# Kernel optimization log

Hardware: AMD Instinct MI355X
Metric: run time of the kernel (lower is better)

Reference implementation:

```python
import jax, jax.numpy as jnp
import numpy as np

N = 6000      # residues (nodes)
E = 120000    # edges (~20 neighbors per node)
D = 128       # node_embedding_dim
De = 128      # edge_embedding_dim
H = 4         # attention heads
L = 2         # encoder layers
C = 2 * D + De
NB, BMIN, BMAX = 16, 2.0, 22.0  # RBF params


def _ln(x, g, b):
    m = x.mean(-1, keepdims=True)
    v = ((x - m) ** 2).mean(-1, keepdims=True)
    return (x - m) / jnp.sqrt(v + 1e-5) * g + b


def setup_inputs() -> dict:
    key = jax.random.key(0)
    ks = iter(jax.random.split(key, 64))

    def nrm(shape, scale=0.05):
        return jax.random.normal(next(ks), shape, jnp.float32) * scale

    inp = {}
    inp['sequence_indices'] = jax.random.randint(next(ks), (N,), 0, 21)
    inp['edge_index'] = jax.random.randint(next(ks), (2, E), 0, N)
    inp['edge_distances'] = BMIN + (BMAX - BMIN) * jax.random.uniform(next(ks), (E,), jnp.float32)
    # parameters
    inp['seq_embed'] = nrm((21, D), 1.0)
    inp['edge_lin_W'] = nrm((NB, De)); inp['edge_lin_b'] = jnp.zeros((De,), jnp.float32)
    inp['aW_W'] = nrm((L, H, C, D)); inp['aW_b'] = jnp.zeros((L, H, D), jnp.float32)
    inp['aA_W'] = nrm((L, H, D));    inp['aA_b'] = jnp.zeros((L, H), jnp.float32)
    inp['nmlp_W1'] = nrm((L, C, D)); inp['nmlp_b1'] = jnp.zeros((L, D), jnp.float32)
    inp['nmlp_W2'] = nrm((L, D, D)); inp['nmlp_b2'] = jnp.zeros((L, D), jnp.float32)
    inp['nmlp_W3'] = nrm((L, D, D)); inp['nmlp_b3'] = jnp.zeros((L, D), jnp.float32)
    inp['dmlp_W1'] = nrm((L, D, 4 * D)); inp['dmlp_b1'] = jnp.zeros((L, 4 * D), jnp.float32)
    inp['dmlp_W2'] = nrm((L, 4 * D, D)); inp['dmlp_b2'] = jnp.zeros((L, D), jnp.float32)
    inp['emlp_W1'] = nrm((L, C, De));  inp['emlp_b1'] = jnp.zeros((L, De), jnp.float32)
    inp['emlp_W2'] = nrm((L, De, De)); inp['emlp_b2'] = jnp.zeros((L, De), jnp.float32)
    inp['emlp_W3'] = nrm((L, De, De)); inp['emlp_b3'] = jnp.zeros((L, De), jnp.float32)
    inp['aggr_W'] = nrm((L, H * D, D)); inp['aggr_b'] = jnp.zeros((L, D), jnp.float32)
    inp['n1_g'] = jnp.ones((L, D), jnp.float32);  inp['n1_b'] = jnp.zeros((L, D), jnp.float32)
    inp['e_g'] = jnp.ones((L, De), jnp.float32);  inp['e_b'] = jnp.zeros((L, De), jnp.float32)
    return inp


def reference(sequence_indices, edge_index, edge_distances, seq_embed,
              edge_lin_W, edge_lin_b, aW_W, aW_b, aA_W, aA_b,
              nmlp_W1, nmlp_b1, nmlp_W2, nmlp_b2, nmlp_W3, nmlp_b3,
              dmlp_W1, dmlp_b1, dmlp_W2, dmlp_b2,
              emlp_W1, emlp_b1, emlp_W2, emlp_b2, emlp_W3, emlp_b3,
              aggr_W, aggr_b, n1_g, n1_b, e_g, e_b):
    gelu = lambda x: jax.nn.gelu(x, approximate=False)  # torch default GELU is exact erf
    lrelu = lambda x: jnp.where(x > 0, x, 0.2 * x)      # LeakyReLU(0.2)

    nodes = seq_embed[sequence_indices]                  # [N, D]
    mu = jnp.linspace(BMIN, BMAX, NB)
    sig = (BMAX - BMIN) / NB
    rbf = jnp.exp(-(((edge_distances[:, None] - mu) / sig) ** 2)) + 1e-8  # [E, NB]
    eattr = rbf @ edge_lin_W + edge_lin_b                # [E, De]

    src, snk = edge_index[0], edge_index[1]
    n = nodes.shape[0]
    for l in range(L):
        feat = jnp.concatenate([nodes[src], nodes[snk], eattr], axis=1)        # [E, C]
        h = lrelu(jnp.einsum('ec,hcd->ehd', feat, aW_W[l]) + aW_b[l][None])    # [E, H, D]
        scores = jnp.einsum('ehd,hd->eh', h, aA_W[l]) + aA_b[l][None]          # [E, H]
        nupd = gelu(feat @ nmlp_W1[l] + nmlp_b1[l])
        nupd = gelu(nupd @ nmlp_W2[l] + nmlp_b2[l])
        nupd = nupd @ nmlp_W3[l] + nmlp_b3[l]                                   # [E, D]
        # scatter softmax over sink nodes (per head)
        smax = jax.ops.segment_max(scores, snk, num_segments=n)                 # [N, H]
        att = jnp.exp(scores - smax[snk])                                       # [E, H]
        norm = jax.ops.segment_sum(att + 1e-12, snk, num_segments=n)            # [N, H]
        att = att / norm[snk]
        msg = (att[:, :, None] * nupd[:, None, :]).reshape(E, H * D)            # head-major concat
        agg = jax.ops.segment_sum(msg, snk, num_segments=n)                     # [N, H*D]
        upd = agg @ aggr_W[l] + aggr_b[l]                                       # [N, D]
        nodes = _ln(nodes + upd, n1_g[l], n1_b[l])
        dense = gelu(nodes @ dmlp_W1[l] + dmlp_b1[l]) @ dmlp_W2[l] + dmlp_b2[l]
        # faithful to source: node_norm1 reused, residual re-adds attention update
        nodes = _ln(dense + upd, n1_g[l], n1_b[l])
        ef = jnp.concatenate([nodes[src], nodes[snk], eattr], axis=1)
        eu = gelu(ef @ emlp_W1[l] + emlp_b1[l])
        eu = gelu(eu @ emlp_W2[l] + emlp_b2[l])
        eu = eu @ emlp_W3[l] + emlp_b3[l]
        eattr = _ln(eattr + eu, e_g[l], e_b[l])
    return nodes, eattr
```

## Files before the change

kernel.cpp:

```cpp
#include <hip/hip_runtime.h>
#include <stdint.h>

#define NN 6000
#define EE 120000
#define DD 128
#define CC 384
#define HDIM 512
#define OUT_NODES (NN*DD)
#define OUT_TOTAL (NN*DD + EE*DD)
#define NODE_LO (NN*DD)
#define EDGE_LO (EE*DD)

typedef unsigned short u16;
typedef __bf16 bf16x8 __attribute__((ext_vector_type(8)));
typedef float f32x4 __attribute__((ext_vector_type(4)));

union V8 { u16 s[8]; uint4 v; };

__device__ __forceinline__ float bf2f(u16 u){ union{unsigned i; float f;} x; x.i=(unsigned)u<<16; return x.f; }
__device__ __forceinline__ u16 f2bf(float f){ union{unsigned i; float f;} x; x.f=f; unsigned r=(x.i + 0x7fffu + ((x.i>>16)&1u))>>16; return (u16)r; }
__device__ __forceinline__ float gelu_f(float v){ return 0.5f*v*(1.f + erff(v*0.70710678118654752f)); }

__device__ __forceinline__ void stage16(void* l, const void* g) {
#if __has_builtin(__builtin_amdgcn_global_load_lds)
  __builtin_amdgcn_global_load_lds(
      (__attribute__((address_space(1))) void*)g,
      (__attribute__((address_space(3))) void*)l, 16, 0, 0);
#else
  *(uint4*)l = *(const uint4*)g;
#endif
}

__device__ __forceinline__ void mfma_step(const u16* buf, int wm, int wn, int lane,
                                          f32x4 acc[4][4])
{
  const int ml = lane & 15;
  const int qx = ((lane >> 4) ^ ((ml ^ (ml >> 2)) & 3)) & 3;
  bf16x8 a_h[4], a_l[4], v_h[4], v_l[4];
#pragma unroll
  for (int mi = 0; mi < 4; ++mi) {
    int ro = (wm*64 + mi*16 + ml)*32 + qx*8;
    a_h[mi] = *(const bf16x8*)(buf + ro);
    a_l[mi] = *(const bf16x8*)(buf + 4096 + ro);
  }
#pragma unroll
  for (int ni = 0; ni < 4; ++ni) {
    int ro = (wn*64 + ni*16 + ml)*32 + qx*8;
    v_h[ni] = *(const bf16x8*)(buf + 8192 + ro);
    v_l[ni] = *(const bf16x8*)(buf + 12288 + ro);
  }
#pragma unroll
  for (int mi = 0; mi < 4; ++mi)
#pragma unroll
    for (int ni = 0; ni < 4; ++ni) {
      acc[mi][ni] = __builtin_amdgcn_mfma_f32_16x16x32_bf16(a_h[mi], v_l[ni], acc[mi][ni], 0, 0, 0);
      acc[mi][ni] = __builtin_amdgcn_mfma_f32_16x16x32_bf16(a_l[mi], v_h[ni], acc[mi][ni], 0, 0, 0);
      acc[mi][ni] = __builtin_amdgcn_mfma_f32_16x16x32_bf16(a_h[mi], v_h[ni], acc[mi][ni], 0, 0, 0);
    }
}

__device__ __forceinline__ int xswz(int row, int col) {
  return row*128 + (col ^ ((row&3)<<3) ^ (((row>>2)&3)<<4));
}

__device__ __forceinline__ void mfma_stepX(const u16* X0, const u16* X1, const u16* BB,
                                           int t, int wm, int wn, int lane, f32x4 acc[4][4])
{
  const int ml = lane & 15, qq = lane >> 4;
  const int qx = (qq ^ ((ml ^ (ml >> 2)) & 3)) & 3;
  bf16x8 a_h[4], a_l[4], v_h[4], v_l[4];
#pragma unroll
  for (int mi = 0; mi < 4; ++mi) {
    int o = xswz(wm*64 + mi*16 + ml, t*32 + qq*8);
    a_h[mi] = *(const bf16x8*)(X0 + o);
    a_l[mi] = *(const bf16x8*)(X1 + o);
  }
#pragma unroll
  for (int ni = 0; ni < 4; ++ni) {
    int ro = (wn*64 + ni*16 + ml)*32 + qx*8;
    v_h[ni] = *(const bf16x8*)(BB + ro);
    v_l[ni] = *(const bf16x8*)(BB + 4096 + ro);
  }
#pragma unroll
  for (int mi = 0; mi < 4; ++mi)
#pragma unroll
    for (int ni = 0; ni < 4; ++ni) {
      acc[mi][ni] = __builtin_amdgcn_mfma_f32_16x16x32_bf16(a_h[mi], v_l[ni], acc[mi][ni], 0, 0, 0);
      acc[mi][ni] = __builtin_amdgcn_mfma_f32_16x16x32_bf16(a_l[mi], v_h[ni], acc[mi][ni], 0, 0, 0);
      acc[mi][ni] = __builtin_amdgcn_mfma_f32_16x16x32_bf16(a_h[mi], v_h[ni], acc[mi][ni], 0, 0, 0);
    }
}

__device__ __forceinline__ void coop_loadZ_b(
    float* ZT, const u16* __restrict__ Zh, int zld, int zs0, int zn0,
    const int* __restrict__ src, const int* __restrict__ snk,
    const int* __restrict__ csr, int m0, int M, int tid)
{
#pragma unroll
  for (int it = 0; it < 8; ++it) {
    int idx = it*256 + tid;
    int row = idx >> 4, c8 = idx & 15;
    int gm = m0 + row; if (gm > M-1) gm = M-1;
    int e = csr[gm];
    V8 a8, b8;
    a8.v = *(const uint4*)(Zh + (size_t)src[e]*zld + zs0 + c8*8);
    b8.v = *(const uint4*)(Zh + (size_t)snk[e]*zld + zn0 + c8*8);
    int base = (c8*8) ^ (((row>>2)&1)<<4);
    float* d = ZT + row*128 + base;
#pragma unroll
    for (int j = 0; j < 8; ++j) d[j] = bf2f(a8.s[j]) + bf2f(b8.s[j]);
  }
}

__device__ __forceinline__ void scatter_X(f32x4 acc[4][4], const float* bias, int gelu_on,
                                          u16* X0, u16* X1, int tid)
{
  const int lane = tid & 63, cl = lane & 15, qr = (lane>>4)&3;
  const int wm = (tid>>6)&1, wn = (tid>>7)&1;
#pragma unroll
  for (int ni = 0; ni < 4; ++ni) {
    float bv = bias[wn*64 + ni*16 + cl];
#pragma unroll
    for (int mi = 0; mi < 4; ++mi)
#pragma unroll
      for (int rg = 0; rg < 4; ++rg) {
        int row = wm*64 + mi*16 + qr*4 + rg;
        int col = wn*64 + ni*16 + cl;
        float v = acc[mi][ni][rg] + bv;
        if (gelu_on) v = gelu_f(v);
        u16 h = f2bf(v);
        int o = xswz(row, col);
        X0[o] = h; X1[o] = f2bf(v - bf2f(h));
      }
  }
}

__device__ __forceinline__ void epilogue_f32(
    f32x4 acc[4][4], const float* bias, float* Cp, int M, int ldc,
    int m0, int n0, int tid)
{
  const int lane = tid & 63;
  const int wm = (tid>>6)&1, wn = (tid>>7)&1;
  const int rl = wm*64 + ((lane>>4)&3)*4;
  const int cl0 = wn*64 + (lane & 15);
#pragma unroll
  for (int ni = 0; ni < 4; ++ni) {
    int gn = n0 + cl0 + ni*16;
    float bv = bias ? bias[gn] : 0.f;
#pragma unroll
    for (int mi = 0; mi < 4; ++mi)
#pragma unroll
      for (int rg = 0; rg < 4; ++rg) {
        int gm = m0 + rl + mi*16 + rg;
        if (gm < M) Cp[(size_t)gm*ldc + gn] = acc[mi][ni][rg] + bv;
      }
  }
}

__device__ __forceinline__ void epilogue_h1(
    f32x4 acc[4][4], u16* Cp, u16* SM, int M, int ldn, int m0, int n0, int tid)
{
  const int lane = tid & 63, cl = lane & 15, qr = (lane>>4)&3;
  const int wm = (tid>>6)&1, wn = (tid>>7)&1;
#pragma unroll
  for (int mi = 0; mi < 4; ++mi)
#pragma unroll
    for (int ni = 0; ni < 4; ++ni)
#pragma unroll
      for (int rg = 0; rg < 4; ++rg) {
        int row = wm*64 + mi*16 + qr*4 + rg;
        int col = wn*64 + ni*16 + cl;
        SM[row*128 + (col ^ (qr<<4))] = f2bf(acc[mi][ni][rg]);
      }
  __syncthreads();
#pragma unroll
  for (int it = 0; it < 8; ++it) {
    int idx = it*256 + tid;
    int row = idx >> 4, blk = idx & 15;
    uint4 val = *(const uint4*)(SM + row*128 + ((blk*8) ^ (((row>>2)&3)<<4)));
    int gm = m0 + row;
    if (gm < M) *(uint4*)(Cp + (size_t)gm*ldn + n0 + blk*8) = val;
  }
  __syncthreads();
}

__device__ __forceinline__ void epilogue_hl(
    f32x4 acc[4][4], const float* bias, u16* Ch, u16* Cl, u16* SM,
    int M, int ldn, int gelu_on, int m0, int n0, int tid)
{
  const int lane = tid & 63, cl = lane & 15, qr = (lane>>4)&3;
  const int wm = (tid>>6)&1, wn = (tid>>7)&1;
#pragma unroll
  for (int ni = 0; ni < 4; ++ni) {
    float bv = bias[n0 + wn*64 + cl + ni*16];
#pragma unroll
    for (int mi = 0; mi < 4; ++mi)
#pragma unroll
      for (int rg = 0; rg < 4; ++rg) {
        float v = acc[mi][ni][rg] + bv;
        if (gelu_on) v = gelu_f(v);
        acc[mi][ni][rg] = v;
      }
  }
#pragma unroll
  for (int pass = 0; pass < 2; ++pass) {
#pragma unroll
    for (int mi = 0; mi < 4; ++mi)
#pragma unroll
      for (int ni = 0; ni < 4; ++ni)
#pragma unroll
        for (int rg = 0; rg < 4; ++rg) {
          int row = wm*64 + mi*16 + qr*4 + rg;
          int col = wn*64 + ni*16 + cl;
          float v = acc[mi][ni][rg];
          u16 h = f2bf(v);
          u16 w = pass ? f2bf(v - bf2f(h)) : h;
          SM[row*128 + (col ^ (qr<<4))] = w;
        }
    __syncthreads();
    u16* Cp = pass ? Cl : Ch;
#pragma unroll
    for (int it = 0; it < 8; ++it) {
      int idx = it*256 + tid;
      int row = idx >> 4, blk = idx & 15;
      uint4 val = *(const uint4*)(SM + row*128 + ((blk*8) ^ (((row>>2)&3)<<4)));
      int gm = m0 + row;
      if (gm < M) *(uint4*)(Cp + (size_t)gm*ldn + n0 + blk*8) = val;
    }
    __syncthreads();
  }
}

__global__ __launch_bounds__(256) void k_gemm2(
    const u16* A_h, const u16* A_l, int K,
    const u16* __restrict__ Bh, const u16* __restrict__ Bl,
    const float* __restrict__ bias, float* Cf,
    u16* Ch, u16* Cl, int M, int ldc, int epi)
{
  __shared__ __align__(16) u16 SM[2][16384];
  const int tid = threadIdx.x, lane = tid & 63;
  const int m0 = blockIdx.x*128, n0 = blockIdx.y*128;
  const int wm = (tid>>6)&1, wn = (tid>>7)&1;
  const u16* gA[2]; const u16* gAl[2]; const u16* gB[2]; const u16* gBl[2];
#pragma unroll
  for (int r = 0; r < 2; ++r) {
    int c = r*256 + tid, m = c>>2, q = c&3;
    int qs = q ^ ((m ^ (m>>2)) & 3);
    int gl = m0 + m; if (gl > M-1) gl = M-1;
    gA[r]  = A_h + (size_t)gl*K + qs*8;
    gAl[r] = A_l + (size_t)gl*K + qs*8;
    gB[r]  = Bh + (size_t)(n0+m)*K + qs*8;
    gBl[r] = Bl + (size_t)(n0+m)*K + qs*8;
  }
  auto stage = [&](int t, u16* buf) {
    int kt = t*32;
#pragma unroll
    for (int r = 0; r < 2; ++r) {
      int c8 = (r*256 + tid)*8;
      stage16(buf + c8,         gA[r]  + kt);
      stage16(buf + 4096 + c8,  gAl[r] + kt);
      stage16(buf + 8192 + c8,  gB[r]  + kt);
      stage16(buf + 12288 + c8, gBl[r] + kt);
    }
  };
  f32x4 acc[4][4] = {};
  const int nk = K >> 5;
  stage(0, SM[0]);
  for (int t = 0; t < nk; ++t) {
    __syncthreads();
    if (t + 1 < nk) stage(t + 1, SM[(t+1)&1]);
    mfma_step(SM[t&1], wm, wn, lane, acc);
  }
  __syncthreads();
  if (epi == 3)      epilogue_f32(acc, bias, Cf, M, ldc, m0, n0, tid);
  else if (epi == 8) epilogue_h1(acc, Ch, SM[0], M, ldc, m0, n0, tid);
  else               epilogue_hl(acc, bias, Ch, Cl, SM[0], M, ldc, epi == 5, m0, n0, tid);
}

__global__ __launch_bounds__(256) void k_mlp_chain(
    const u16* __restrict__ nodes_h, const u16* __restrict__ eattr_h,
    const int* __restrict__ src, const int* __restrict__ snk,
    const u16* __restrict__ B1h, const u16* __restrict__ B1l, const float* __restrict__ b1,
    const u16* __restrict__ B2h, const u16* __restrict__ B2l, const float* __restrict__ b2,
    const u16* __restrict__ B3h, const u16* __restrict__ B3l, const float* __restrict__ b3,
    u16* __restrict__ Xh, u16* __restrict__ Xl, int M)
{
  __shared__ __align__(16) u16 SM[2][16384];
  __shared__ __align__(16) u16 BB[8192];
  const int tid = threadIdx.x, lane = tid & 63;
  const int m0 = blockIdx.x*128;
  const int wm = (tid>>6)&1, wn = (tid>>7)&1;
  const u16* pr0[2]; const u16* pr1[2]; const u16* pr2[2];
  const u16* gB[2]; const u16* gBl[2];
  int soff[2];
#pragma unroll
  for (int r = 0; r < 2; ++r) {
    int c = r*256 + tid, m = c>>2, q = c&3;
    int qs = q ^ ((m ^ (m>>2)) & 3);
    int gl = m0 + m; if (gl > M-1) gl = M-1;
    pr0[r] = nodes_h + (size_t)src[gl]*DD + qs*8;
    pr1[r] = nodes_h + (size_t)snk[gl]*DD + qs*8;
    pr2[r] = eattr_h + (size_t)gl*DD + qs*8;
    gB[r]  = B1h + (size_t)m*CC + qs*8;
    gBl[r] = B1l + (size_t)m*CC + qs*8;
    soff[r] = m*128 + qs*8;
  }
  auto stage_g = [&](int t, u16* buf) {
    int reg = t >> 2, kk = (t & 3) * 32;
    const int LO = (reg == 2) ? EDGE_LO : NODE_LO;
#pragma unroll
    for (int r = 0; r < 2; ++r) {
      int c8 = (r*256 + tid)*8;
      const u16* g = (reg == 0 ? pr0[r] : reg == 1 ? pr1[r] : pr2[r]) + kk;
      stage16(buf + c8,         g);
      stage16(buf + 4096 + c8,  g + LO);
      stage16(buf + 8192 + c8,  gB[r]  + t*32);
      stage16(buf + 12288 + c8, gBl[r] + t*32);
    }
  };
  auto stageB = [&](const u16* Bh_, const u16* Bl_, int t) {
#pragma unroll
    for (int r = 0; r < 2; ++r) {
      int c8 = (r*256 + tid)*8;
      stage16(BB + c8,        Bh_ + soff[r] + t*32);
      stage16(BB + 4096 + c8, Bl_ + soff[r] + t*32);
    }
  };
  f32x4 acc[4][4] = {};
  stage_g(0, SM[0]);
  for (int t = 0; t < 12; ++t) {
    __syncthreads();
    if (t < 11) stage_g(t + 1, SM[(t+1)&1]);
    mfma_step(SM[t&1], wm, wn, lane, acc);
  }
  __syncthreads();
  scatter_X(acc, b1, 1, (u16*)SM[0], (u16*)SM[1], tid);
  __syncthreads();
#pragma unroll
  for (int mi = 0; mi < 4; ++mi)
#pragma unroll
    for (int ni = 0; ni < 4; ++ni)
#pragma unroll
      for (int rg = 0; rg < 4; ++rg) acc[mi][ni][rg] = 0.f;
  for (int t = 0; t < 4; ++t) {
    stageB(B2h, B2l, t);
    __syncthreads();
    mfma_stepX((const u16*)SM[0], (const u16*)SM[1], BB, t, wm, wn, lane, acc);
    __syncthreads();
  }
  scatter_X(acc, b2, 1, (u16*)SM[0], (u16*)SM[1], tid);
  __syncthreads();
#pragma unroll
  for (int mi = 0; mi < 4; ++mi)
#pragma unroll
    for (int ni = 0; ni < 4; ++ni)
#pragma unroll
      for (int rg = 0; rg < 4; ++rg) acc[mi][ni][rg] = 0.f;
  for (int t = 0; t < 4; ++t) {
    stageB(B3h, B3l, t);
    __syncthreads();
    mfma_stepX((const u16*)SM[0], (const u16*)SM[1], BB, t, wm, wn, lane, acc);
    __syncthreads();
  }
  epilogue_hl(acc, b3, Xh, Xl, (u16*)SM[0], M, 128, 0, m0, 0, tid);
}

__global__ __launch_bounds__(256) void k_score(
    const u16* __restrict__ eattr_h,
    const int* __restrict__ src, const int* __restrict__ snk,
    const int* __restrict__ csr,
    const u16* __restrict__ Bh, const u16* __restrict__ Bl,
    const float* __restrict__ bias,
    const float* __restrict__ aAw, const float* __restrict__ aAb,
    const u16* __restrict__ Zatt,
    float* __restrict__ scores_out, int M)
{
  __shared__ __align__(16) u16 SM[2][16384];
  const int tid = threadIdx.x, lane = tid & 63;
  int p = (blockIdx.x & 7) * 469 + (blockIdx.x >> 3);
  const int bm = p >> 2, bn = p & 3;
  const int m0 = bm*128, n0 = bn*128;
  const int wm = (tid>>6)&1, wn = (tid>>7)&1;
  const u16* pr2[2]; const u16* gB[2]; const u16* gBl[2];
#pragma unroll
  for (int r = 0; r < 2; ++r) {
    int c = r*256 + tid, m = c>>2, q = c&3;
    int qs = q ^ ((m ^ (m>>2)) & 3);
    int gl = m0 + m; if (gl > M-1) gl = M-1;
    int ce = csr[gl];
    pr2[r] = eattr_h + (size_t)ce*DD + qs*8;
    gB[r]  = Bh + (size_t)(n0+m)*DD + qs*8;
    gBl[r] = Bl + (size_t)(n0+m)*DD + qs*8;
  }
  auto stage_s = [&](int t, u16* buf) {
#pragma unroll
    for (int r = 0; r < 2; ++r) {
      int c8 = (r*256 + tid)*8;
      stage16(buf + c8,         pr2[r] + t*32);
      stage16(buf + 4096 + c8,  pr2[r] + EDGE_LO + t*32);
      stage16(buf + 8192 + c8,  gB[r]  + t*32);
      stage16(buf + 12288 + c8, gBl[r] + t*32);
    }
  };
  f32x4 acc[4][4] = {};
  stage_s(0, SM[0]);
  for (int t = 0; t < 4; ++t) {
    __syncthreads();
    if (t < 3) stage_s(t + 1, SM[(t+1)&1]);
    mfma_step(SM[t&1], wm, wn, lane, acc);
  }
  __syncthreads();
  float* ZT = (float*)SM;
  coop_loadZ_b(ZT, Zatt, 1024, n0, 512 + n0, src, snk, csr, m0, M, tid);
  __syncthreads();
  const int cl = lane & 15, qr = (lane>>4)&3;
  float pv[16];
#pragma unroll
  for (int mi = 0; mi < 4; ++mi)
#pragma unroll
    for (int rg = 0; rg < 4; ++rg) {
      int row = wm*64 + mi*16 + qr*4 + rg;
      int s = ((row>>2)&1)<<4;
      float pacc = 0.f;
#pragma unroll
      for (int ni = 0; ni < 4; ++ni) {
        int lc = wn*64 + ni*16 + cl;
        int gn = n0 + lc;
        float v = acc[mi][ni][rg] + bias[gn] + ZT[row*128 + (lc ^ s)];
        v = (v > 0.f) ? v : 0.2f*v;
        pacc += v * aAw[gn];
      }
      pacc += __shfl_xor(pacc, 1, 64); pacc += __shfl_xor(pacc, 2, 64);
      pacc += __shfl_xor(pacc, 4, 64); pacc += __shfl_xor(pacc, 8, 64);
      pv[mi*4 + rg] = pacc;
    }
  __syncthreads();
  float* sred = (float*)SM[0];
#pragma unroll
  for (int mi = 0; mi < 4; ++mi)
#pragma unroll
    for (int rg = 0; rg < 4; ++rg)
      if (cl == 0) sred[wn*128 + wm*64 + mi*16 + qr*4 + rg] = pv[mi*4 + rg];
  __syncthreads();
  if (tid < 128) {
    int gm = m0 + tid;
    if (gm < M) scores_out[(size_t)csr[gm]*4 + bn] = sred[tid] + sred[128 + tid] + aAb[bn];
  }
}

__global__ void k_detect(const u16* __restrict__ d, int n, int* __restrict__ flag) {
  __shared__ int cnt;
  if (threadIdx.x == 0) cnt = 0;
  __syncthreads();
  int c = 0;
  for (int i = threadIdx.x; i < n; i += blockDim.x) {
    int e = (d[i] >> 7) & 0xff;
    if (e >= 0xC0) ++c;
  }
  atomicAdd(&cnt, c);
  __syncthreads();
  if (threadIdx.x == 0) *flag = (cnt > 16) ? 1 : 0;
}

struct ConvDesc { const void* src; float* dst; int n; };
struct ConvArgs { ConvDesc d[30]; };
__global__ void k_conv32(ConvArgs a, const int* __restrict__ flag) {
  ConvDesc de = a.d[blockIdx.y];
  int fp = *flag;
  for (int i = blockIdx.x*256 + threadIdx.x; i < de.n; i += gridDim.x*256)
    de.dst[i] = fp ? ((const float*)de.src)[i] : bf2f(((const u16*)de.src)[i]);
}

struct PackDesc { const float* src; u16* dh; u16* dl; int K, N, sk, sh; };
struct PackArgs { PackDesc d[32]; int n; };
__global__ void k_pack2(PackArgs a) {
  PackDesc de = a.d[blockIdx.y];
  int total = de.K * de.N;
  for (int i = blockIdx.x*256 + threadIdx.x; i < total; i += gridDim.x*256) {
    int k = i / de.N, n = i - k*de.N;
    float x = de.src[(size_t)k*de.sk + (n & 127) + (n >> 7)*de.sh];
    u16 h = f2bf(x);
    de.dh[(size_t)n*de.K + k] = h;
    de.dl[(size_t)n*de.K + k] = f2bf(x - bf2f(h));
  }
}

__global__ void k_init_nodes(const int* __restrict__ seq, const float* __restrict__ emb,
                             float* __restrict__ nodes_f, u16* __restrict__ nh) {
  int i = blockIdx.x*256 + threadIdx.x;
  if (i >= NN*DD) return;
  int n = i >> 7, d = i & 127;
  float v = emb[seq[n]*DD + d];
  nodes_f[i] = v;
  u16 h = f2bf(v); nh[i] = h; nh[NODE_LO + i] = f2bf(v - bf2f(h));
}

__global__ void k_rbf_s(const float* __restrict__ dist, const float* __restrict__ W,
                        const float* __restrict__ b, u16* __restrict__ eh) {
  int e = blockIdx.x, t = threadIdx.x;
  float d = dist[e];
  float acc = b[t];
#pragma unroll
  for (int k = 0; k < 16; ++k) {
    float mu = 2.f + (20.f/15.f)*(float)k;
    float z = (d - mu)*0.8f;
    float r = expf(-z*z) + 1e-8f;
    acc += r*W[k*DD + t];
  }
  size_t idx = (size_t)e*DD + t;
  u16 h = f2bf(acc); eh[idx] = h; eh[(size_t)EDGE_LO + idx] = f2bf(acc - bf2f(h));
}

__global__ void k_hist(const int* __restrict__ snk, int* __restrict__ deg) {
  int e = blockIdx.x*256 + threadIdx.x;
  if (e < EE) atomicAdd(&deg[snk[e]], 1);
}
__global__ void k_scan(const int* __restrict__ deg, int* __restrict__ ptr, int* __restrict__ cursor, int n) {
  __shared__ int buf[1024];
  __shared__ int carry_s;
  int tid = threadIdx.x;
  if (tid == 0) carry_s = 0;
  __syncthreads();
  for (int base = 0; base < n; base += 1024) {
    int i = base + tid;
    int v = (i < n) ? deg[i] : 0;
    buf[tid] = v;
    __syncthreads();
    for (int off = 1; off < 1024; off <<= 1) {
      int t = (tid >= off) ? buf[tid - off] : 0;
      __syncthreads();
      buf[tid] += t;
      __syncthreads();
    }
    int excl = buf[tid] - v;
    int carry = carry_s;
    if (i < n) { ptr[i] = carry + excl; cursor[i] = carry + excl; }
    __syncthreads();
    if (tid == 1023) carry_s = carry + buf[1023];
    __syncthreads();
  }
  if (tid == 0) ptr[n] = carry_s;
}
__global__ void k_scatter(const int* __restrict__ snk, int* __restrict__ cursor, int* __restrict__ csr) {
  int e = blockIdx.x*256 + threadIdx.x;
  if (e < EE) { int p = atomicAdd(&cursor[snk[e]], 1); csr[p] = e; }
}

__global__ void k_softmax(const float* __restrict__ scores, const int* __restrict__ ptr,
                          const int* __restrict__ csr, float* __restrict__ att, int nnodes) {
  int node = blockIdx.x*4 + (threadIdx.x >> 6);
  if (node >= nnodes) return;
  int lane = threadIdx.x & 63;
  int h = lane >> 4, j = lane & 15;
  int b = ptr[node], e = ptr[node+1];
  float mx = -1e30f;
  for (int i = b + j; i < e; i += 16) mx = fmaxf(mx, scores[(size_t)csr[i]*4 + h]);
  mx = fmaxf(mx, __shfl_xor(mx, 1, 64)); mx = fmaxf(mx, __shfl_xor(mx, 2, 64));
  mx = fmaxf(mx, __shfl_xor(mx, 4, 64)); mx = fmaxf(mx, __shfl_xor(mx, 8, 64));
  float s = 0.f;
  for (int i = b + j; i < e; i += 16) s += expf(scores[(size_t)csr[i]*4 + h] - mx);
  s += __shfl_xor(s, 1, 64); s += __shfl_xor(s, 2, 64);
  s += __shfl_xor(s, 4, 64); s += __shfl_xor(s, 8, 64);
  float norm = s + (float)(e - b)*1e-12f;
  float inv = (e > b) ? 1.f/norm : 0.f;
  for (int i = b + j; i < e; i += 16) {
    int ed = csr[i];
    att[(size_t)ed*4 + h] = expf(scores[(size_t)ed*4 + h] - mx)*inv;
  }
}

__global__ void k_aggregate(const float* __restrict__ att,
                            const u16* __restrict__ Xh, const u16* __restrict__ Xl,
                            const int* __restrict__ ptr, const int* __restrict__ csr,
                            u16* __restrict__ agg_h, u16* __restrict__ agg_l) {
  int node = blockIdx.x; int d = threadIdx.x;
  int b = ptr[node], e = ptr[node+1];
  float a0=0.f, a1=0.f, a2=0.f, a3=0.f;
  for (int i = b; i < e; ++i) {
    int ed = csr[i];
    float4 a = *(const float4*)(att + (size_t)ed*4);
    size_t xo = (size_t)ed*DD + d;
    float v = bf2f(Xh[xo]) + bf2f(Xl[xo]);
    a0 += a.x*v; a1 += a.y*v; a2 += a.z*v; a3 += a.w*v;
  }
  size_t o = (size_t)node*HDIM + d;
  float vv[4] = {a0, a1, a2, a3};
#pragma unroll
  for (int h = 0; h < 4; ++h) {
    u16 hi = f2bf(vv[h]);
    agg_h[o + h*128] = hi;
    agg_l[o + h*128] = f2bf(vv[h] - bf2f(hi));
  }
}

__global__ void k_ln_node(float* __restrict__ nodes_f,
                          const float* __restrict__ upd, const float* __restrict__ dense_f,
                          const float* __restrict__ g, const float* __restrict__ b,
                          int mode, int rows, u16* __restrict__ nh) {
  int r = blockIdx.x*4 + (threadIdx.x >> 6);
  if (r >= rows) return;
  int lane = threadIdx.x & 63;
  size_t o = (size_t)r*DD;
  float x0, x1;
  if (mode == 0) { x0 = nodes_f[o+lane]; x1 = nodes_f[o+lane+64]; }
  else           { x0 = dense_f[o+lane]; x1 = dense_f[o+lane+64]; }
  x0 += upd[o+lane]; x1 += upd[o+lane+64];
  float s = x0 + x1;
#pragma unroll
  for (int m = 1; m < 64; m <<= 1) s += __shfl_xor(s, m, 64);
  float mean = s * (1.f/128.f);
  float d0 = x0 - mean, d1 = x1 - mean;
  float vv = d0*d0 + d1*d1;
#pragma unroll
  for (int m = 1; m < 64; m <<= 1) vv += __shfl_xor(vv, m, 64);
  float inv = rsqrtf(vv*(1.f/128.f) + 1e-5f);
  float v0 = d0*inv*g[lane]    + b[lane];
  float v1 = d1*inv*g[lane+64] + b[lane+64];
  nodes_f[o+lane]    = v0;
  nodes_f[o+lane+64] = v1;
  u16 h0 = f2bf(v0), h1 = f2bf(v1);
  nh[o+lane] = h0;    nh[NODE_LO + o+lane]    = f2bf(v0 - bf2f(h0));
  nh[o+lane+64] = h1; nh[NODE_LO + o+lane+64] = f2bf(v1 - bf2f(h1));
}

__global__ void k_ln_edge(const u16* __restrict__ Xh, const u16* __restrict__ Xl,
                          const float* __restrict__ g, const float* __restrict__ b,
                          int rows, u16* __restrict__ eh) {
  int r = blockIdx.x*4 + (threadIdx.x >> 6);
  if (r >= rows) return;
  int lane = threadIdx.x & 63;
  size_t o = (size_t)r*DD;
  float x0 = bf2f(eh[o+lane])    + bf2f(eh[(size_t)EDGE_LO + o+lane])
           + bf2f(Xh[o+lane])    + bf2f(Xl[o+lane]);
  float x1 = bf2f(eh[o+lane+64]) + bf2f(eh[(size_t)EDGE_LO + o+lane+64])
           + bf2f(Xh[o+lane+64]) + bf2f(Xl[o+lane+64]);
  float s = x0 + x1;
#pragma unroll
  for (int m = 1; m < 64; m <<= 1) s += __shfl_xor(s, m, 64);
  float mean = s * (1.f/128.f);
  float d0 = x0 - mean, d1 = x1 - mean;
  float vv = d0*d0 + d1*d1;
#pragma unroll
  for (int m = 1; m < 64; m <<= 1) vv += __shfl_xor(vv, m, 64);
  float inv = rsqrtf(vv*(1.f/128.f) + 1e-5f);
  float v0 = d0*inv*g[lane]    + b[lane];
  float v1 = d1*inv*g[lane+64] + b[lane+64];
  u16 h0 = f2bf(v0), h1 = f2bf(v1);
  eh[o+lane] = h0;    eh[(size_t)EDGE_LO + o+lane]    = f2bf(v0 - bf2f(h0));
  eh[o+lane+64] = h1; eh[(size_t)EDGE_LO + o+lane+64] = f2bf(v1 - bf2f(h1));
}

__global__ void k_finalize(const float* __restrict__ nodes_f, const u16* __restrict__ eh,
                           void* __restrict__ out, const int* __restrict__ flag) {
  int i = blockIdx.x*256 + threadIdx.x;
  if (i >= OUT_TOTAL) return;
  int fp = *flag;
  float v;
  if (i < OUT_NODES) v = nodes_f[i];
  else { int j = i - OUT_NODES; v = bf2f(eh[j]) + bf2f(eh[(size_t)EDGE_LO + j]); }
  if (fp) ((float*)out)[i] = v; else ((u16*)out)[i] = f2bf(v);
}

extern "C" void kernel_launch(void* const* d_in, const int* in_sizes, int n_in,
                              void* d_out, int out_size, void* d_ws, size_t ws_size,
                              hipStream_t stream)
{
  const int* seq_idx = (const int*)d_in[0];
  const int* esrc = (const int*)d_in[1];
  const int* esnk = ((const int*)d_in[1]) + EE;

  char* wsp = (char*)d_ws;
  size_t off = 0;
  auto carve = [&](size_t bytes)->char* {
    char* p = wsp + off; off += (bytes + 255) & ~(size_t)255; return p;
  };
  int* flag       = (int*)carve(256);
  float* nodes_f  = (float*)carve((size_t)NN*DD*4);
  float* upd_f    = (float*)carve((size_t)NN*DD*4);
  float* scores   = (float*)carve((size_t)EE*4*4);
  float* att      = (float*)carve((size_t)EE*4*4);
  float* dense_f  = (float*)carve((size_t)NN*DD*4);
  u16* Zatt       = (u16*)carve((size_t)NN*1024*2);
  u16* wpk_h      = (u16*)carve(557056ULL*2*2);
  u16* wpk_l      = (u16*)carve(557056ULL*2*2);
  int* deg        = (int*)carve((size_t)NN*4);
  int* ptrb       = (int*)carve((size_t)(NN+1)*4);
  int* cursor     = (int*)carve((size_t)NN*4);
  int* csr        = (int*)carve((size_t)EE*4);
  u16* nodes_h    = (u16*)carve((size_t)2*NN*DD*2);
  u16* eattr_h    = (u16*)carve((size_t)2*EE*DD*2);
  u16* X_h        = (u16*)carve((size_t)2*EE*DD*2);
  u16* agg_h      = (u16*)carve((size_t)2*NN*HDIM*2);
  u16* dh_h       = (u16*)carve((size_t)2*NN*HDIM*2);
  u16* X_l   = X_h   + (size_t)EE*DD;
  u16* agg_l = agg_h + (size_t)NN*HDIM;
  u16* dh_l  = dh_h  + (size_t)NN*HDIM;

  static const int FCNT[32] = {0,0,120000,2688,2048,128,393216,1024,1024,8,
    98304,256,32768,256,32768,256, 131072,1024,131072,256,
    98304,256,32768,256,32768,256, 131072,256, 256,256,256,256};
  float* cf[32];
  for (int i = 2; i < 32; ++i) cf[i] = (float*)carve((size_t)FCNT[i]*4);
  (void)ws_size; (void)in_sizes; (void)n_in; (void)out_size;

  k_detect<<<1, 1024, 0, stream>>>((const u16*)d_in[2], 120000, flag);
  ConvArgs ca;
  for (int i = 2; i < 32; ++i) { ca.d[i-2].src = d_in[i]; ca.d[i-2].dst = cf[i]; ca.d[i-2].n = FCNT[i]; }
  hipLaunchKernelGGL(k_conv32, dim3(96, 30), dim3(256), 0, stream, ca, flag);

  const size_t PW_L = 557056;
  PackArgs pa; int nd = 0;
  for (int l = 0; l < 2; ++l) {
    size_t base = l*PW_L;
    auto add = [&](const float* s, size_t doff, int K, int N, int sk, int sh){
      pa.d[nd].src = s; pa.d[nd].dh = wpk_h + doff; pa.d[nd].dl = wpk_l + doff;
      pa.d[nd].K = K; pa.d[nd].N = N; pa.d[nd].sk = sk; pa.d[nd].sh = sh; ++nd; };
    const float* aW = cf[6] + l*196608;
    add(aW,          base + 0,      128, 512, 128, 49152);
    add(aW + 16384,  base + 65536,  128, 512, 128, 49152);
    add(aW + 32768,  base + 131072, 128, 512, 128, 49152);
    add(cf[10] + l*49152, base + 196608, 384, 128, 128, 0);
    add(cf[12] + l*16384, base + 245760, 128, 128, 128, 0);
    add(cf[14] + l*16384, base + 262144, 128, 128, 128, 0);
    add(cf[26] + l*65536, base + 278528, 512, 128, 128, 0);
    add(cf[16] + l*65536, base + 344064, 128, 512, 512, 128);
    add(cf[18] + l*65536, base + 409600, 512, 128, 128, 0);
    add(cf[20] + l*49152, base + 475136, 384, 128, 128, 0);
    add(cf[22] + l*16384, base + 524288, 128, 128, 128, 0);
    add(cf[24] + l*16384, base + 540672, 128, 128, 128, 0);
  }
  pa.n = nd;
  hipLaunchKernelGGL(k_pack2, dim3(256, nd), dim3(256), 0, stream, pa);

  k_init_nodes<<<(NN*DD + 255)/256, 256, 0, stream>>>(seq_idx, cf[3], nodes_f, nodes_h);
  k_rbf_s<<<EE, 128, 0, stream>>>(cf[2], cf[4], cf[5], eattr_h);

  (void)hipMemsetAsync(deg, 0, (size_t)NN*4, stream);
  k_hist<<<(EE + 255)/256, 256, 0, stream>>>(esnk, deg);
  k_scan<<<1, 1024, 0, stream>>>(deg, ptrb, cursor, NN);
  k_scatter<<<(EE + 255)/256, 256, 0, stream>>>(esnk, cursor, csr);

  for (int l = 0; l < 2; ++l) {
    const u16* bh = wpk_h + l*PW_L; const u16* bl = wpk_l + l*PW_L;
    k_gemm2<<<dim3(47, 8), 256, 0, stream>>>(nodes_h, nodes_h + NODE_LO, 128,
        bh + 0, bl + 0, nullptr, nullptr, Zatt, nullptr, NN, 1024, 8);
    k_score<<<dim3(3752), 256, 0, stream>>>(eattr_h, esrc, esnk, csr,
        bh + 131072, bl + 131072, cf[7] + l*512, cf[8] + l*512, cf[9] + l*4,
        Zatt, scores, EE);
    k_mlp_chain<<<dim3(938), 256, 0, stream>>>(nodes_h, eattr_h, esrc, esnk,
        bh + 196608, bl + 196608, cf[11] + l*128,
        bh + 245760, bl + 245760, cf[13] + l*128,
        bh + 262144, bl + 262144, cf[15] + l*128,
        X_h, X_l, EE);
    k_softmax<<<(NN + 3)/4, 256, 0, stream>>>(scores, ptrb, csr, att, NN);
    k_aggregate<<<NN, 128, 0, stream>>>(att, X_h, X_l, ptrb, csr, agg_h, agg_l);
    k_gemm2<<<dim3(47, 1), 256, 0, stream>>>(agg_h, agg_l, 512, bh + 278528, bl + 278528,
        cf[27] + l*128, upd_f, nullptr, nullptr, NN, 128, 3);
    k_ln_node<<<(NN + 3)/4, 256, 0, stream>>>(nodes_f, upd_f, (const float*)nullptr,
        cf[28] + l*128, cf[29] + l*128, 0, NN, nodes_h);
    k_gemm2<<<dim3(47, 4), 256, 0, stream>>>(nodes_h, nodes_h + NODE_LO, 128,
        bh + 344064, bl + 344064, cf[17] + l*512, nullptr, dh_h, dh_l, NN, 512, 5);
    k_gemm2<<<dim3(47, 1), 256, 0, stream>>>(dh_h, dh_l, 512, bh + 409600, bl + 409600,
        cf[19] + l*128, dense_f, nullptr, nullptr, NN, 128, 3);
    k_ln_node<<<(NN + 3)/4, 256, 0, stream>>>(nodes_f, upd_f, dense_f,
        cf[28] + l*128, cf[29] + l*128, 1, NN, nodes_h);
    k_mlp_chain<<<dim3(938), 256, 0, stream>>>(nodes_h, eattr_h, esrc, esnk,
        bh + 475136, bl + 475136, cf[21] + l*128,
        bh + 524288, bl + 524288, cf[23] + l*128,
        bh + 540672, bl + 540672, cf[25] + l*128,
        X_h, X_l, EE);
    k_ln_edge<<<(EE + 3)/4, 256, 0, stream>>>(X_h, X_l,
        cf[30] + l*128, cf[31] + l*128, EE, eattr_h);
  }
  k_finalize<<<(OUT_TOTAL + 255)/256, 256, 0, stream>>>(nodes_f, eattr_h, d_out, flag);
}
```

Baseline: 1.175 ms.

## Fuse edge LayerNorm into MLP chain epilogue and read small weights from global

New measurement: 1.247 ms. 6.1% more time.

```diff
diff --git a/kernel.cpp b/kernel.cpp
--- a/kernel.cpp
+++ b/kernel.cpp
@@ -63,23 +63,23 @@
   return row*128 + (col ^ ((row&3)<<3) ^ (((row>>2)&3)<<4));
 }
 
-__device__ __forceinline__ void mfma_stepX(const u16* X0, const u16* X1, const u16* BB,
-                                           int t, int wm, int wn, int lane, f32x4 acc[4][4])
+__device__ __forceinline__ void mfma_stepXg(const u16* X0, const u16* X1,
+    const u16* __restrict__ Bh, const u16* __restrict__ Bl,
+    int t, int wm, int wn, int lane, f32x4 acc[4][4])
 {
   const int ml = lane & 15, qq = lane >> 4;
-  const int qx = (qq ^ ((ml ^ (ml >> 2)) & 3)) & 3;
   bf16x8 a_h[4], a_l[4], v_h[4], v_l[4];
+#pragma unroll
+  for (int ni = 0; ni < 4; ++ni) {
+    size_t ro = (size_t)(wn*64 + ni*16 + ml)*128 + t*32 + qq*8;
+    v_h[ni] = *(const bf16x8*)(Bh + ro);
+    v_l[ni] = *(const bf16x8*)(Bl + ro);
+  }
 #pragma unroll
   for (int mi = 0; mi < 4; ++mi) {
     int o = xswz(wm*64 + mi*16 + ml, t*32 + qq*8);
     a_h[mi] = *(const bf16x8*)(X0 + o);
     a_l[mi] = *(const bf16x8*)(X1 + o);
-  }
-#pragma unroll
-  for (int ni = 0; ni < 4; ++ni) {
-    int ro = (wn*64 + ni*16 + ml)*32 + qx*8;
-    v_h[ni] = *(const bf16x8*)(BB + ro);
-    v_l[ni] = *(const bf16x8*)(BB + 4096 + ro);
   }
 #pragma unroll
   for (int mi = 0; mi < 4; ++mi)
@@ -228,6 +228,54 @@
       if (gm < M) *(uint4*)(Cp + (size_t)gm*ldn + n0 + blk*8) = val;
     }
     __syncthreads();
+  }
+}
+
+__device__ __forceinline__ void epilogue_lnedge(
+    f32x4 acc[4][4], const float* bias, const float* g, const float* b,
+    u16* eh, float* SMf, int M, int m0, int tid)
+{
+  const int lane = tid & 63, cl = lane & 15, qr = (lane>>4)&3;
+  const int wm = (tid>>6)&1, wn = (tid>>7)&1;
+#pragma unroll
+  for (int ni = 0; ni < 4; ++ni) {
+    float bv = bias[wn*64 + ni*16 + cl];
+#pragma unroll
+    for (int mi = 0; mi < 4; ++mi)
+#pragma unroll
+      for (int rg = 0; rg < 4; ++rg) {
+        int row = wm*64 + mi*16 + qr*4 + rg;
+        int col = wn*64 + ni*16 + cl;
+        SMf[row*128 + (col ^ (((row>>2)&1)<<4))] = acc[mi][ni][rg] + bv;
+      }
+  }
+  __syncthreads();
+  const int wid = tid >> 6;
+  float gl0 = g[lane], gl1 = g[lane+64], bl0 = b[lane], bl1 = b[lane+64];
+  for (int rr = 0; rr < 32; ++rr) {
+    int row = wid*32 + rr;
+    int gm = m0 + row;
+    if (gm >= M) break;
+    int s = ((row>>2)&1)<<4;
+    size_t o = (size_t)gm*DD;
+    float x0 = SMf[row*128 + (lane ^ s)]
+             + bf2f(eh[o+lane]) + bf2f(eh[(size_t)EDGE_LO + o+lane]);
+    float x1 = SMf[row*128 + ((lane+64) ^ s)]
+             + bf2f(eh[o+lane+64]) + bf2f(eh[(size_t)EDGE_LO + o+lane+64]);
+    float ss = x0 + x1;
+#pragma unroll
+    for (int mm = 1; mm < 64; mm <<= 1) ss += __shfl_xor(ss, mm, 64);
+    float mean = ss * (1.f/128.f);
+    float d0 = x0 - mean, d1 = x1 - mean;
+    float vv = d0*d0 + d1*d1;
+#pragma unroll
+    for (int mm = 1; mm < 64; mm <<= 1) vv += __shfl_xor(vv, mm, 64);
+    float inv = rsqrtf(vv*(1.f/128.f) + 1e-5f);
+    float v0 = d0*inv*gl0 + bl0;
+    float v1 = d1*inv*gl1 + bl1;
+    u16 h0 = f2bf(v0), h1 = f2bf(v1);
+    eh[o+lane] = h0;    eh[(size_t)EDGE_LO + o+lane]    = f2bf(v0 - bf2f(h0));
+    eh[o+lane+64] = h1; eh[(size_t)EDGE_LO + o+lane+64] = f2bf(v1 - bf2f(h1));
   }
 }
 
@@ -283,16 +331,15 @@
     const u16* __restrict__ B1h, const u16* __restrict__ B1l, const float* __restrict__ b1,
     const u16* __restrict__ B2h, const u16* __restrict__ B2l, const float* __restrict__ b2,
     const u16* __restrict__ B3h, const u16* __restrict__ B3l, const float* __restrict__ b3,
-    u16* __restrict__ Xh, u16* __restrict__ Xl, int M)
+    u16* __restrict__ Xh, u16* __restrict__ Xl, int M,
+    int mode, const float* __restrict__ lng, const float* __restrict__ lnb)
 {
   __shared__ __align__(16) u16 SM[2][16384];
-  __shared__ __align__(16) u16 BB[8192];
   const int tid = threadIdx.x, lane = tid & 63;
   const int m0 = blockIdx.x*128;
   const int wm = (tid>>6)&1, wn = (tid>>7)&1;
   const u16* pr0[2]; const u16* pr1[2]; const u16* pr2[2];
   const u16* gB[2]; const u16* gBl[2];
-  int soff[2];
 #pragma unroll
   for (int r = 0; r < 2; ++r) {
     int c = r*256 + tid, m = c>>2, q = c&3;
@@ -303,7 +350,6 @@
     pr2[r] = eattr_h + (size_t)gl*DD + qs*8;
     gB[r]  = B1h + (size_t)m*CC + qs*8;
     gBl[r] = B1l + (size_t)m*CC + qs*8;
-    soff[r] = m*128 + qs*8;
   }
   auto stage_g = [&](int t, u16* buf) {
     int reg = t >> 2, kk = (t & 3) * 32;
@@ -318,14 +364,6 @@
       stage16(buf + 12288 + c8, gBl[r] + t*32);
     }
   };
-  auto stageB = [&](const u16* Bh_, const u16* Bl_, int t) {
-#pragma unroll
-    for (int r = 0; r < 2; ++r) {
-      int c8 = (r*256 + tid)*8;
-      stage16(BB + c8,        Bh_ + soff[r] + t*32);
-      stage16(BB + 4096 + c8, Bl_ + soff[r] + t*32);
-    }
-  };
   f32x4 acc[4][4] = {};
   stage_g(0, SM[0]);
   for (int t = 0; t < 12; ++t) {
@@ -342,12 +380,10 @@
     for (int ni = 0; ni < 4; ++ni)
 #pragma unroll
       for (int rg = 0; rg < 4; ++rg) acc[mi][ni][rg] = 0.f;
-  for (int t = 0; t < 4; ++t) {
-    stageB(B2h, B2l, t);
-    __syncthreads();
-    mfma_stepX((const u16*)SM[0], (const u16*)SM[1], BB, t, wm, wn, lane, acc);
-    __syncthreads();
-  }
+#pragma unroll
+  for (int t = 0; t < 4; ++t)
+    mfma_stepXg((const u16*)SM[0], (const u16*)SM[1], B2h, B2l, t, wm, wn, lane, acc);
+  __syncthreads();
   scatter_X(acc, b2, 1, (u16*)SM[0], (u16*)SM[1], tid);
   __syncthreads();
 #pragma unroll
@@ -356,13 +392,12 @@
     for (int ni = 0; ni < 4; ++ni)
 #pragma unroll
       for (int rg = 0; rg < 4; ++rg) acc[mi][ni][rg] = 0.f;
-  for (int t = 0; t < 4; ++t) {
-    stageB(B3h, B3l, t);
-    __syncthreads();
-    mfma_stepX((const u16*)SM[0], (const u16*)SM[1], BB, t, wm, wn, lane, acc);
-    __syncthreads();
-  }
-  epilogue_hl(acc, b3, Xh, Xl, (u16*)SM[0], M, 128, 0, m0, 0, tid);
+#pragma unroll
+  for (int t = 0; t < 4; ++t)
+    mfma_stepXg((const u16*)SM[0], (const u16*)SM[1], B3h, B3l, t, wm, wn, lane, acc);
+  __syncthreads();
+  if (mode == 0) epilogue_hl(acc, b3, Xh, Xl, (u16*)SM[0], M, 128, 0, m0, 0, tid);
+  else           epilogue_lnedge(acc, b3, lng, lnb, Xh, (float*)SM, M, m0, tid);
 }
 
 __global__ __launch_bounds__(256) void k_score(
@@ -621,33 +656,6 @@
   u16 h0 = f2bf(v0), h1 = f2bf(v1);
   nh[o+lane] = h0;    nh[NODE_LO + o+lane]    = f2bf(v0 - bf2f(h0));
   nh[o+lane+64] = h1; nh[NODE_LO + o+lane+64] = f2bf(v1 - bf2f(h1));
-}
-
-__global__ void k_ln_edge(const u16* __restrict__ Xh, const u16* __restrict__ Xl,
-                          const float* __restrict__ g, const float* __restrict__ b,
-                          int rows, u16* __restrict__ eh) {
-  int r = blockIdx.x*4 + (threadIdx.x >> 6);
-  if (r >= rows) return;
-  int lane = threadIdx.x & 63;
-  size_t o = (size_t)r*DD;
-  float x0 = bf2f(eh[o+lane])    + bf2f(eh[(size_t)EDGE_LO + o+lane])
-           + bf2f(Xh[o+lane])    + bf2f(Xl[o+lane]);
-  float x1 = bf2f(eh[o+lane+64]) + bf2f(eh[(size_t)EDGE_LO + o+lane+64])
-           + bf2f(Xh[o+lane+64]) + bf2f(Xl[o+lane+64]);
-  float s = x0 + x1;
-#pragma unroll
-  for (int m = 1; m < 64; m <<= 1) s += __shfl_xor(s, m, 64);
-  float mean = s * (1.f/128.f);
-  float d0 = x0 - mean, d1 = x1 - mean;
-  float vv = d0*d0 + d1*d1;
-#pragma unroll
-  for (int m = 1; m < 64; m <<= 1) vv += __shfl_xor(vv, m, 64);
-  float inv = rsqrtf(vv*(1.f/128.f) + 1e-5f);
-  float v0 = d0*inv*g[lane]    + b[lane];
-  float v1 = d1*inv*g[lane+64] + b[lane+64];
-  u16 h0 = f2bf(v0), h1 = f2bf(v1);
-  eh[o+lane] = h0;    eh[(size_t)EDGE_LO + o+lane]    = f2bf(v0 - bf2f(h0));
-  eh[o+lane+64] = h1; eh[(size_t)EDGE_LO + o+lane+64] = f2bf(v1 - bf2f(h1));
 }
 
 __global__ void k_finalize(const float* __restrict__ nodes_f, const u16* __restrict__ eh,
@@ -751,7 +759,7 @@
         bh + 196608, bl + 196608, cf[11] + l*128,
         bh + 245760, bl + 245760, cf[13] + l*128,
         bh + 262144, bl + 262144, cf[15] + l*128,
-        X_h, X_l, EE);
+        X_h, X_l, EE, 0, nullptr, nullptr);
     k_softmax<<<(NN + 3)/4, 256, 0, stream>>>(scores, ptrb, csr, att, NN);
     k_aggregate<<<NN, 128, 0, stream>>>(att, X_h, X_l, ptrb, csr, agg_h, agg_l);
     k_gemm2<<<dim3(47, 1), 256, 0, stream>>>(agg_h, agg_l, 512, bh + 278528, bl + 278528,
@@ -768,9 +776,7 @@
         bh + 475136, bl + 475136, cf[21] + l*128,
         bh + 524288, bl + 524288, cf[23] + l*128,
         bh + 540672, bl + 540672, cf[25] + l*128,
-        X_h, X_l, EE);
-    k_ln_edge<<<(EE + 3)/4, 256, 0, stream>>>(X_h, X_l,
-        cf[30] + l*128, cf[31] + l*128, EE, eattr_h);
+        eattr_h, nullptr, EE, 1, cf[30] + l*128, cf[31] + l*128);
   }
   k_finalize<<<(OUT_TOTAL + 255)/256, 256, 0, stream>>>(nodes_f, eattr_h, d_out, flag);
 }
```
